# Optimization experiments

Measured on AMD Instinct MI355X. Metric: run time of the kernel, lower is better.

## Reference

```python
import jax, jax.numpy as jnp
import numpy as np

N_NODES = 20000   # nodes
IN_DEG = 8        # fixed in-degree -> E = N*D edges, T = E*D triplets
MSG = 64          # message_size


def _build_indices():
    rng = np.random.default_rng(0)
    E = N_NODES * IN_DEG
    # edge e: row[e] -> col[e]; node j's incoming edges are j*D : (j+1)*D
    row = rng.integers(0, N_NODES, size=E).astype(np.int32)          # source j of edge (j->i)
    # triplets of edge e=(j->i): all edges k->j, i.e. incoming edges of row[e]
    idx_kj = (row[:, None] * IN_DEG + np.arange(IN_DEG, dtype=np.int32)[None, :]).reshape(-1)
    idx_ji = np.repeat(np.arange(E, dtype=np.int32), IN_DEG)
    idx_j = np.repeat(row, IN_DEG)   # pooled-to node for each triplet
    return idx_kj, idx_ji, idx_j, E


def setup_inputs() -> dict:
    idx_kj, idx_ji, idx_j, E = _build_indices()
    key = jax.random.key(0)
    ks = jax.random.split(key, 8)
    s1 = 1.0 / np.sqrt(2 * MSG)
    s2 = 1.0 / np.sqrt(MSG)
    return {
        "messages": jax.random.normal(ks[0], (E, MSG), jnp.float32),
        "r": jax.random.normal(ks[1], (E, 2), jnp.float32),
        "W1": jax.random.uniform(ks[2], (2 * MSG, MSG), jnp.float32, -s1, s1),
        "b1": jax.random.uniform(ks[3], (MSG,), jnp.float32, -s1, s1),
        "W2": jax.random.uniform(ks[4], (MSG, MSG), jnp.float32, -s2, s2),
        "b2": jax.random.uniform(ks[5], (MSG,), jnp.float32, -s2, s2),
        "W3": jax.random.uniform(ks[6], (MSG, 1), jnp.float32, -s2, s2),
        "b3": jax.random.uniform(ks[7], (1,), jnp.float32, -s2, s2),
        "idx_kj": jnp.asarray(idx_kj),
        "idx_ji": jnp.asarray(idx_ji),
        "idx_j": jnp.asarray(idx_j),
        "num_nodes": N_NODES,
    }


def reference(messages, r, W1, b1, W2, b2, W3, b3, idx_kj, idx_ji, idx_j, num_nodes):
    # gather triplet messages and run the 3-layer MLP (Linear/Softplus/Linear/Softplus/Linear)
    h = jnp.concatenate([messages[idx_kj], messages[idx_ji]], axis=1)  # [T, 2M]
    h = jax.nn.softplus(h @ W1 + b1)
    h = jax.nn.softplus(h @ W2 + b2)
    m_ijk = h @ W3 + b3                                                # [T, 1]
    # dyad[t,k,j] = r[idx_ji][t,k] * r[idx_kj][t,j]  (einsum 'ij,ik->ikj')
    rk = r[idx_kj]                                                     # [T, 2]
    rj = r[idx_ji]                                                     # [T, 2]
    dyad = (rj[:, :, None] * rk[:, None, :]).reshape(-1, 4)            # [T, 4]
    temp = m_ijk * dyad                                                # [T, 4]
    # global_mean_pool over idx_j
    s = jax.ops.segment_sum(temp, idx_j, num_segments=num_nodes)       # [N, 4]
    cnt = jax.ops.segment_sum(jnp.ones((temp.shape[0],), temp.dtype), idx_j,
                              num_segments=num_nodes)
    out = s / jnp.maximum(cnt, 1.0)[:, None]
    return out.reshape(-1, 2, 2)
```

## Files before the change

kernel.cpp:

```cpp
#include <hip/hip_runtime.h>

typedef _Float16 half8 __attribute__((ext_vector_type(8)));
typedef __fp16 fp16x2 __attribute__((ext_vector_type(2)));
typedef float floatx4 __attribute__((ext_vector_type(4)));

#define MSGW 64
#define DEG 8

__device__ __forceinline__ float softplus_f(float x) {
    float ax = __builtin_fabsf(x);
    float t  = __builtin_amdgcn_exp2f(-1.44269504089f * ax);
    float l  = 0.69314718056f * __builtin_amdgcn_logf(1.0f + t);
    return fmaxf(x, 0.0f) + l;
}

__device__ __forceinline__ half8 cvt8(const float* p) {
    float4 x = *(const float4*)p;
    float4 y = *(const float4*)(p + 4);
    fp16x2 p0 = __builtin_amdgcn_cvt_pkrtz(x.x, x.y);
    fp16x2 p1 = __builtin_amdgcn_cvt_pkrtz(x.z, x.w);
    fp16x2 p2 = __builtin_amdgcn_cvt_pkrtz(y.x, y.y);
    fp16x2 p3 = __builtin_amdgcn_cvt_pkrtz(y.z, y.w);
    half8 h;
    h[0] = (_Float16)p0[0]; h[1] = (_Float16)p0[1];
    h[2] = (_Float16)p1[0]; h[3] = (_Float16)p1[1];
    h[4] = (_Float16)p2[0]; h[5] = (_Float16)p2[1];
    h[6] = (_Float16)p3[0]; h[7] = (_Float16)p3[1];
    return h;
}

__global__ __launch_bounds__(256, 3)
void triplet_mlp_kernel(const float* __restrict__ messages,
                        const float* __restrict__ r2,
                        const float* __restrict__ W1, const float* __restrict__ b1,
                        const float* __restrict__ W2, const float* __restrict__ b2,
                        const float* __restrict__ W3, const float* __restrict__ b3,
                        const int* __restrict__ idx_kj,
                        float* __restrict__ sacc, float* __restrict__ cnt,
                        int nChunks)
{
    __shared__ _Float16 lw1x[16 * 512];
    __shared__ _Float16 lw2x[8 * 512];
    __shared__ float lb1[64], lb2[64], lw3[64];
    __shared__ _Float16 lh[4][16 * 72];

    const int tid = threadIdx.x;
    for (int i = tid; i < 128 * 64; i += 256) {
        int k = i >> 6, n = i & 63;
        int ks = k >> 5, q = (k >> 3) & 3, j = k & 7;
        int nt = n >> 4, s = n & 15;
        lw1x[(nt * 4 + ks) * 512 + (q * 16 + s) * 8 + j] = (_Float16)W1[i];
    }
    for (int i = tid; i < 64 * 64; i += 256) {
        int k = i >> 6, n = i & 63;
        int ks = k >> 5, q = (k >> 3) & 3, j = k & 7;
        int nt = n >> 4, s = n & 15;
        lw2x[(nt * 2 + ks) * 512 + (q * 16 + s) * 8 + j] = (_Float16)W2[i];
    }
    if (tid < 64) { lb1[tid] = b1[tid]; lb2[tid] = b2[tid]; lw3[tid] = W3[tid]; }
    __syncthreads();

    const int wave = tid >> 6;
    const int lane = tid & 63;
    const int s = lane & 15;
    const int q = lane >> 4;
    const float b3v = b3[0];
    const int T = nChunks * 64;
    const int stride = gridDim.x * 64;

    _Float16* myh = lh[wave];

    int t = blockIdx.x * 64 + wave * 16 + s;
    int kj = (t < T) ? idx_kj[t] : 0;

    for (int chunk = blockIdx.x; chunk < nChunks; chunk += gridDim.x) {
        const int t_next = t + stride;
        const int kj_next = idx_kj[(t_next < T) ? t_next : 0];

        const int ji = t >> 3;
        const int jn = kj >> 3;

        const float* mk = messages + (size_t)kj * MSGW + q * 8;
        const float* mj = messages + (size_t)ji * MSGW + q * 8;
        half8 afr[4];
        afr[0] = cvt8(mk);
        afr[1] = cvt8(mk + 32);
        afr[2] = cvt8(mj);
        afr[3] = cvt8(mj + 32);

        const float rk0 = r2[(size_t)kj * 2];
        const float rk1 = r2[(size_t)kj * 2 + 1];

        floatx4 acc[4];
#pragma unroll
        for (int nt = 0; nt < 4; ++nt) {
            float bv = lb1[nt * 16 + s];
            floatx4 iv = {bv, bv, bv, bv};
            acc[nt] = iv;
        }
#pragma unroll
        for (int ks = 0; ks < 4; ++ks)
#pragma unroll
            for (int nt = 0; nt < 4; ++nt) {
                half8 bf = *(const half8*)&lw1x[(nt * 4 + ks) * 512 + lane * 8];
                acc[nt] = __builtin_amdgcn_mfma_f32_16x16x32_f16(afr[ks], bf, acc[nt], 0, 0, 0);
            }

#pragma unroll
        for (int nt = 0; nt < 4; ++nt)
#pragma unroll
            for (int rr = 0; rr < 4; ++rr)
                myh[(q * 4 + rr) * 72 + nt * 16 + s] = (_Float16)softplus_f(acc[nt][rr]);
        __asm__ volatile("s_waitcnt lgkmcnt(0)" ::: "memory");

        half8 a2[2];
        a2[0] = *(const half8*)&myh[s * 72 + q * 8];
        a2[1] = *(const half8*)&myh[s * 72 + 32 + q * 8];
        __asm__ volatile("" ::: "memory");

        floatx4 acc2[4];
#pragma unroll
        for (int nt = 0; nt < 4; ++nt) {
            float bv = lb2[nt * 16 + s];
            floatx4 iv = {bv, bv, bv, bv};
            acc2[nt] = iv;
        }
#pragma unroll
        for (int ks = 0; ks < 2; ++ks)
#pragma unroll
            for (int nt = 0; nt < 4; ++nt) {
                half8 bf = *(const half8*)&lw2x[(nt * 2 + ks) * 512 + lane * 8];
                acc2[nt] = __builtin_amdgcn_mfma_f32_16x16x32_f16(a2[ks], bf, acc2[nt], 0, 0, 0);
            }

        float part[4];
#pragma unroll
        for (int rr = 0; rr < 4; ++rr) {
            float p = 0.0f;
#pragma unroll
            for (int nt = 0; nt < 4; ++nt)
                p += softplus_f(acc2[nt][rr]) * lw3[nt * 16 + s];
            part[rr] = p;
        }
#pragma unroll
        for (int mask = 1; mask < 16; mask <<= 1)
#pragma unroll
            for (int rr = 0; rr < 4; ++rr)
                part[rr] += __shfl_xor(part[rr], mask, 16);

        const int srcl = (s >> 2) << 4;
        float mr[4];
#pragma unroll
        for (int rr = 0; rr < 4; ++rr)
            mr[rr] = __shfl(part[rr], srcl, 64);
        const int rsel = s & 3;
        float m_mine = mr[0];
        m_mine = (rsel == 1) ? mr[1] : m_mine;
        m_mine = (rsel == 2) ? mr[2] : m_mine;
        m_mine = (rsel == 3) ? mr[3] : m_mine;
        m_mine += b3v;

        float c = m_mine * ((q & 1) ? rk1 : rk0);
        c += __shfl_xor(c, 1, 16);
        c += __shfl_xor(c, 2, 16);
        c += __shfl_xor(c, 4, 16);

        if ((s & 7) == 0) {
            const int aa = q >> 1, bb = q & 1;
            const float rj = r2[(size_t)ji * 2 + aa];
            atomicAdd(&sacc[(size_t)jn * 4 + aa * 2 + bb], rj * c);
            if (q == 0) atomicAdd(&cnt[jn], 8.0f);
        }

        t = t_next;
        kj = kj_next;
    }
}

__global__ void finalize_kernel(const float* __restrict__ sacc, const float* __restrict__ cnt,
                                float* __restrict__ out, int n4) {
    int i = blockIdx.x * 256 + threadIdx.x;
    if (i < n4) {
        float c = cnt[i >> 2];
        out[i] = sacc[i] / fmaxf(c, 1.0f);
    }
}

extern "C" void kernel_launch(void* const* d_in, const int* in_sizes, int n_in,
                              void* d_out, int out_size, void* d_ws, size_t ws_size,
                              hipStream_t stream) {
    const float* messages = (const float*)d_in[0];
    const float* r2       = (const float*)d_in[1];
    const float* W1       = (const float*)d_in[2];
    const float* b1       = (const float*)d_in[3];
    const float* W2       = (const float*)d_in[4];
    const float* b2       = (const float*)d_in[5];
    const float* W3       = (const float*)d_in[6];
    const float* b3       = (const float*)d_in[7];
    const int* idx_kj     = (const int*)d_in[8];

    const int T = in_sizes[8];
    const int N = out_size / 4;
    float* sacc = (float*)d_ws;
    float* cntp = sacc + (size_t)N * 4;

    (void)hipMemsetAsync(d_ws, 0, (size_t)N * 5 * sizeof(float), stream);

    const int nChunks = T / 64;
    int grid = nChunks < 4096 ? nChunks : 4096;
    triplet_mlp_kernel<<<grid, 256, 0, stream>>>(messages, r2, W1, b1, W2, b2, W3, b3,
                                                 idx_kj, sacc, cntp, nChunks);

    const int n4 = N * 4;
    finalize_kernel<<<(n4 + 255) / 256, 256, 0, stream>>>(sacc, cntp, (float*)d_out, n4);
}
```

Measured before the change: 216.1 us.

## Transpose MFMA operands to keep activations in registers and fold softplus scaling into weights

Swaps the MFMA operand roles so weights are the A operand and triplet messages the B operand. Each lane then holds one triplet's hidden features across rows, so the layer-1 outputs are packed straight into the layer-2 B fragment with a permuted W2 layout, with no LDS round-trip. The final W3 dot product collapses to two cross-quad shuffles instead of a 16-lane butterfly plus a broadcast. Log2e and ln2 are folded into W1, b1, b2 and W3 so softplus runs in base 2 without extra multiplies, and launch bounds rise to 6 blocks per CU, which tightens the register budget and risks spills.

```diff
diff --git a/kernel.cpp b/kernel.cpp
--- a/kernel.cpp
+++ b/kernel.cpp
@@ -7,11 +7,9 @@
 #define MSGW 64
 #define DEG 8
 
-__device__ __forceinline__ float softplus_f(float x) {
-    float ax = __builtin_fabsf(x);
-    float t  = __builtin_amdgcn_exp2f(-1.44269504089f * ax);
-    float l  = 0.69314718056f * __builtin_amdgcn_logf(1.0f + t);
-    return fmaxf(x, 0.0f) + l;
+__device__ __forceinline__ float softplus_l2(float z) {
+    float e = __builtin_amdgcn_exp2f(-__builtin_fabsf(z));
+    return fmaxf(z, 0.0f) + __builtin_amdgcn_logf(1.0f + e);
 }
 
 __device__ __forceinline__ half8 cvt8(const float* p) {
@@ -29,7 +27,7 @@
     return h;
 }
 
-__global__ __launch_bounds__(256, 3)
+__global__ __launch_bounds__(256, 6)
 void triplet_mlp_kernel(const float* __restrict__ messages,
                         const float* __restrict__ r2,
                         const float* __restrict__ W1, const float* __restrict__ b1,
@@ -39,28 +37,35 @@
                         float* __restrict__ sacc, float* __restrict__ cnt,
                         int nChunks)
 {
-    __shared__ _Float16 lw1x[16 * 512];
-    __shared__ _Float16 lw2x[8 * 512];
-    __shared__ float lb1[64], lb2[64], lw3[64];
-    __shared__ _Float16 lh[4][16 * 72];
+    __shared__ __align__(16) _Float16 lw1x[16 * 512];
+    __shared__ __align__(16) _Float16 lw2x[8 * 512];
+    __shared__ __align__(16) float lb1[64];
+    __shared__ __align__(16) float lb2[64];
+    __shared__ __align__(16) float lw3f[64];
+
+    const float LOG2E = 1.44269504088896340736f;
+    const float LN2   = 0.69314718055994530942f;
 
     const int tid = threadIdx.x;
     for (int i = tid; i < 128 * 64; i += 256) {
         int k = i >> 6, n = i & 63;
         int ks = k >> 5, q = (k >> 3) & 3, j = k & 7;
         int nt = n >> 4, s = n & 15;
-        lw1x[(nt * 4 + ks) * 512 + (q * 16 + s) * 8 + j] = (_Float16)W1[i];
+        lw1x[(nt * 4 + ks) * 512 + (q * 16 + s) * 8 + j] = (_Float16)(W1[i] * LOG2E);
     }
     for (int i = tid; i < 64 * 64; i += 256) {
-        int k = i >> 6, n = i & 63;
-        int ks = k >> 5, q = (k >> 3) & 3, j = k & 7;
-        int nt = n >> 4, s = n & 15;
-        lw2x[(nt * 2 + ks) * 512 + (q * 16 + s) * 8 + j] = (_Float16)W2[i];
-    }
-    if (tid < 64) { lb1[tid] = b1[tid]; lb2[tid] = b2[tid]; lw3[tid] = W3[tid]; }
+        int h = i >> 6, n = i & 63;
+        int ks2 = h >> 5, q = (h >> 2) & 3, j = ((h >> 4) & 1) * 4 + (h & 3);
+        int nt2 = n >> 4, s = n & 15;
+        lw2x[(nt2 * 2 + ks2) * 512 + (q * 16 + s) * 8 + j] = (_Float16)W2[i];
+    }
+    if (tid < 64) {
+        lb1[tid] = b1[tid] * LOG2E;
+        lb2[tid] = b2[tid] * LOG2E;
+        lw3f[tid] = W3[tid] * LN2;
+    }
     __syncthreads();
 
-    const int wave = tid >> 6;
     const int lane = tid & 63;
     const int s = lane & 15;
     const int q = lane >> 4;
@@ -68,9 +73,7 @@
     const int T = nChunks * 64;
     const int stride = gridDim.x * 64;
 
-    _Float16* myh = lh[wave];
-
-    int t = blockIdx.x * 64 + wave * 16 + s;
+    int t = blockIdx.x * 64 + (tid >> 6) * 16 + s;
     int kj = (t < T) ? idx_kj[t] : 0;
 
     for (int chunk = blockIdx.x; chunk < nChunks; chunk += gridDim.x) {
@@ -82,85 +85,68 @@
 
         const float* mk = messages + (size_t)kj * MSGW + q * 8;
         const float* mj = messages + (size_t)ji * MSGW + q * 8;
-        half8 afr[4];
-        afr[0] = cvt8(mk);
-        afr[1] = cvt8(mk + 32);
-        afr[2] = cvt8(mj);
-        afr[3] = cvt8(mj + 32);
-
-        const float rk0 = r2[(size_t)kj * 2];
-        const float rk1 = r2[(size_t)kj * 2 + 1];
+        half8 bfr[4];
+        bfr[0] = cvt8(mk);
+        bfr[1] = cvt8(mk + 32);
+        bfr[2] = cvt8(mj);
+        bfr[3] = cvt8(mj + 32);
+
+        const float rk = r2[(size_t)kj * 2 + (q & 1)];
 
         floatx4 acc[4];
 #pragma unroll
+        for (int nt = 0; nt < 4; ++nt)
+            acc[nt] = *(const floatx4*)&lb1[nt * 16 + q * 4];
+#pragma unroll
+        for (int ks = 0; ks < 4; ++ks)
+#pragma unroll
+            for (int nt = 0; nt < 4; ++nt) {
+                half8 af = *(const half8*)&lw1x[(nt * 4 + ks) * 512 + lane * 8];
+                acc[nt] = __builtin_amdgcn_mfma_f32_16x16x32_f16(af, bfr[ks], acc[nt], 0, 0, 0);
+            }
+
+        fp16x2 p[4][2];
+#pragma unroll
         for (int nt = 0; nt < 4; ++nt) {
-            float bv = lb1[nt * 16 + s];
-            floatx4 iv = {bv, bv, bv, bv};
-            acc[nt] = iv;
-        }
-#pragma unroll
-        for (int ks = 0; ks < 4; ++ks)
-#pragma unroll
-            for (int nt = 0; nt < 4; ++nt) {
-                half8 bf = *(const half8*)&lw1x[(nt * 4 + ks) * 512 + lane * 8];
-                acc[nt] = __builtin_amdgcn_mfma_f32_16x16x32_f16(afr[ks], bf, acc[nt], 0, 0, 0);
+            float u0 = softplus_l2(acc[nt][0]);
+            float u1 = softplus_l2(acc[nt][1]);
+            float u2 = softplus_l2(acc[nt][2]);
+            float u3 = softplus_l2(acc[nt][3]);
+            p[nt][0] = __builtin_amdgcn_cvt_pkrtz(u0, u1);
+            p[nt][1] = __builtin_amdgcn_cvt_pkrtz(u2, u3);
+        }
+        union U8 { fp16x2 h2[4]; half8 h8; };
+        U8 c0, c1;
+        c0.h2[0] = p[0][0]; c0.h2[1] = p[0][1]; c0.h2[2] = p[1][0]; c0.h2[3] = p[1][1];
+        c1.h2[0] = p[2][0]; c1.h2[1] = p[2][1]; c1.h2[2] = p[3][0]; c1.h2[3] = p[3][1];
+
+        floatx4 acc2[4];
+#pragma unroll
+        for (int nt2 = 0; nt2 < 4; ++nt2)
+            acc2[nt2] = *(const floatx4*)&lb2[nt2 * 16 + q * 4];
+#pragma unroll
+        for (int ks2 = 0; ks2 < 2; ++ks2) {
+            half8 bf = ks2 ? c1.h8 : c0.h8;
+#pragma unroll
+            for (int nt2 = 0; nt2 < 4; ++nt2) {
+                half8 af = *(const half8*)&lw2x[(nt2 * 2 + ks2) * 512 + lane * 8];
+                acc2[nt2] = __builtin_amdgcn_mfma_f32_16x16x32_f16(af, bf, acc2[nt2], 0, 0, 0);
             }
-
-#pragma unroll
-        for (int nt = 0; nt < 4; ++nt)
+        }
+
+        float msum = 0.0f;
+#pragma unroll
+        for (int nt2 = 0; nt2 < 4; ++nt2) {
+            floatx4 w3q = *(const floatx4*)&lw3f[nt2 * 16 + q * 4];
 #pragma unroll
             for (int rr = 0; rr < 4; ++rr)
-                myh[(q * 4 + rr) * 72 + nt * 16 + s] = (_Float16)softplus_f(acc[nt][rr]);
-        __asm__ volatile("s_waitcnt lgkmcnt(0)" ::: "memory");
-
-        half8 a2[2];
-        a2[0] = *(const half8*)&myh[s * 72 + q * 8];
-        a2[1] = *(const half8*)&myh[s * 72 + 32 + q * 8];
-        __asm__ volatile("" ::: "memory");
-
-        floatx4 acc2[4];
-#pragma unroll
-        for (int nt = 0; nt < 4; ++nt) {
-            float bv = lb2[nt * 16 + s];
-            floatx4 iv = {bv, bv, bv, bv};
-            acc2[nt] = iv;
-        }
-#pragma unroll
-        for (int ks = 0; ks < 2; ++ks)
-#pragma unroll
-            for (int nt = 0; nt < 4; ++nt) {
-                half8 bf = *(const half8*)&lw2x[(nt * 2 + ks) * 512 + lane * 8];
-                acc2[nt] = __builtin_amdgcn_mfma_f32_16x16x32_f16(a2[ks], bf, acc2[nt], 0, 0, 0);
-            }
-
-        float part[4];
-#pragma unroll
-        for (int rr = 0; rr < 4; ++rr) {
-            float p = 0.0f;
-#pragma unroll
-            for (int nt = 0; nt < 4; ++nt)
-                p += softplus_f(acc2[nt][rr]) * lw3[nt * 16 + s];
-            part[rr] = p;
-        }
-#pragma unroll
-        for (int mask = 1; mask < 16; mask <<= 1)
-#pragma unroll
-            for (int rr = 0; rr < 4; ++rr)
-                part[rr] += __shfl_xor(part[rr], mask, 16);
-
-        const int srcl = (s >> 2) << 4;
-        float mr[4];
-#pragma unroll
-        for (int rr = 0; rr < 4; ++rr)
-            mr[rr] = __shfl(part[rr], srcl, 64);
-        const int rsel = s & 3;
-        float m_mine = mr[0];
-        m_mine = (rsel == 1) ? mr[1] : m_mine;
-        m_mine = (rsel == 2) ? mr[2] : m_mine;
-        m_mine = (rsel == 3) ? mr[3] : m_mine;
-        m_mine += b3v;
-
-        float c = m_mine * ((q & 1) ? rk1 : rk0);
+                msum += softplus_l2(acc2[nt2][rr]) * w3q[rr];
+        }
+        msum += __shfl_xor(msum, 16, 64);
+        msum += __shfl_xor(msum, 32, 64);
+        const float m = msum + b3v;
+
+        float c = m * rk;
         c += __shfl_xor(c, 1, 16);
         c += __shfl_xor(c, 2, 16);
         c += __shfl_xor(c, 4, 16);
```

Result: slower. 592.4 us (+174.2%).
